# Optimization experiments

Measured on AMD Instinct MI355X. Metric: run time of the kernel, lower is better.

Reference implementation:

```python
import jax, jax.numpy as jnp
import numpy as np

N = 50000   # num nodes
R = 8       # num relations
E = 800000  # num edges
IN, HID, OUT = 128, 128, 64


def rgcn_layer(x, src, dst, etype, W, root, bias):
    """PyG-style RGCNConv: per-relation mean aggregation + root weight + bias.
    x: [N, I], W: [R, I, O], root: [I, O], bias: [O]."""
    O = W.shape[-1]
    # transform node features once per relation: [R, N, O]
    xr = jnp.einsum('ni,rio->rno', x, W)
    # per-edge message = relation-specific transform of source node
    m = xr[etype, src]                      # [E, O] gather
    # mean-aggregate per (relation, dst) pair, then sum over relations
    idx = etype * N + dst                   # combined segment id in [0, R*N)
    s = jax.ops.segment_sum(m, idx, num_segments=R * N)          # [R*N, O]
    c = jax.ops.segment_sum(jnp.ones_like(etype, dtype=m.dtype), idx,
                            num_segments=R * N)                   # [R*N]
    agg = (s / jnp.maximum(c, 1.0)[:, None]).reshape(R, N, O).sum(axis=0)
    return agg + x @ root + bias


def setup_inputs() -> dict:
    key = jax.random.key(0)
    ks = jax.random.split(key, 16)
    x = jax.random.normal(ks[0], (N, IN), dtype=jnp.float32)
    edge_index = jax.random.randint(ks[1], (2, E), 0, N, dtype=jnp.int32)
    edge_type = jax.random.randint(ks[2], (E,), 0, R, dtype=jnp.int32)
    dims = [(IN, HID), (HID, HID), (HID, HID), (HID, OUT)]
    inp = {"x": x, "edge_index": edge_index, "edge_type": edge_type}
    for li, (i, o) in enumerate(dims):
        sc = 1.0 / np.sqrt(i)
        inp[f"W{li+1}"] = jax.random.normal(ks[3 + 3 * li], (R, i, o), dtype=jnp.float32) * sc
        inp[f"root{li+1}"] = jax.random.normal(ks[4 + 3 * li], (i, o), dtype=jnp.float32) * sc
        inp[f"b{li+1}"] = jnp.zeros((o,), dtype=jnp.float32)
    return inp


def reference(x, edge_index, edge_type,
              W1, root1, b1, W2, root2, b2,
              W3, root3, b3, W4, root4, b4):
    src, dst = edge_index[0], edge_index[1]
    h = jax.nn.relu(rgcn_layer(x, src, dst, edge_type, W1, root1, b1))
    h = jax.nn.relu(rgcn_layer(h, src, dst, edge_type, W2, root2, b2))
    h = jax.nn.relu(rgcn_layer(h, src, dst, edge_type, W3, root3, b3))
    h = rgcn_layer(h, src, dst, edge_type, W4, root4, b4)
    return jax.nn.log_softmax(h, axis=1)
```

## Files before the change

### kernel.cpp

```cpp
#include <hip/hip_runtime.h>
#include <math.h>

#define NN 50000
#define RR 8
#define EE 800000
#define RN 400000
#define DIN 128
#define K1 1024
#define KTOT 1152
#define NBLK 391

#define OFF_U    0UL
#define OFF_HB0  102400000UL
#define OFF_HB1  115200000UL
#define OFF_XB   128000000UL
#define OFF_LG   140800000UL
#define OFF_WT   153600000UL
#define OFF_OFFS 154780160UL
#define OFF_CUR  156380288UL
#define OFF_SRT  157980288UL
#define OFF_BS   161180288UL
#define WS_NEED  161184384UL

typedef short bf16x8 __attribute__((ext_vector_type(8)));
typedef float f32x4 __attribute__((ext_vector_type(4)));

__device__ __forceinline__ unsigned f2bf(float f) {
    unsigned x = __float_as_uint(f);
    return (x + 0x7fffu + ((x >> 16) & 1u)) >> 16;
}
__device__ __forceinline__ float bflo(unsigned p) { return __uint_as_float(p << 16); }
__device__ __forceinline__ float bfhi(unsigned p) { return __uint_as_float(p & 0xffff0000u); }

__global__ void k_cvt(const float* __restrict__ x, ushort* __restrict__ xb) {
    int i = blockIdx.x * 256 + threadIdx.x;
    if (i >= NN * 32) return;
    float4 v = ((const float4*)x)[i];
    ushort4 o;
    o.x = (ushort)f2bf(v.x); o.y = (ushort)f2bf(v.y);
    o.z = (ushort)f2bf(v.z); o.w = (ushort)f2bf(v.w);
    ((ushort4*)xb)[i] = o;
}

__global__ void k_wt(const float* __restrict__ W, const float* __restrict__ Rt,
                     ushort* __restrict__ WT, int O) {
    int o = blockIdx.x;
    for (int k = threadIdx.x; k < KTOT; k += 256) {
        float v = (k < K1)
            ? W[(size_t)(k >> 7) * 128 * O + (size_t)(k & 127) * O + o]
            : Rt[(size_t)(k - K1) * O + o];
        WT[(size_t)o * KTOT + k] = (ushort)f2bf(v);
    }
}

__global__ void k_hist(const int* __restrict__ ei, const int* __restrict__ et,
                       int* __restrict__ hist) {
    int e = blockIdx.x * blockDim.x + threadIdx.x;
    if (e >= EE) return;
    atomicAdd(&hist[ei[EE + e] * RR + et[e]], 1);
}

__global__ void k_scan1(const int* __restrict__ hist, int* __restrict__ offs,
                        int* __restrict__ bsums) {
    __shared__ int tmp[1024];
    int tid = threadIdx.x;
    int g = blockIdx.x * 1024 + tid;
    int v = (g < RN) ? hist[g] : 0;
    tmp[tid] = v;
    __syncthreads();
    for (int off = 1; off < 1024; off <<= 1) {
        int t = tmp[tid];
        if (tid >= off) t += tmp[tid - off];
        __syncthreads();
        tmp[tid] = t;
        __syncthreads();
    }
    if (g < RN) offs[g] = tmp[tid] - v;
    if (tid == 1023) bsums[blockIdx.x] = tmp[1023];
}

__global__ void k_scan2(int* __restrict__ bsums) {
    __shared__ int tmp[1024];
    int tid = threadIdx.x;
    int v = (tid < NBLK) ? bsums[tid] : 0;
    tmp[tid] = v;
    __syncthreads();
    for (int off = 1; off < 1024; off <<= 1) {
        int t = tmp[tid];
        if (tid >= off) t += tmp[tid - off];
        __syncthreads();
        tmp[tid] = t;
        __syncthreads();
    }
    if (tid < NBLK) bsums[tid] = tmp[tid] - v;
}

__global__ void k_scan3(int* __restrict__ offs, const int* __restrict__ bsums) {
    int g = blockIdx.x * 1024 + threadIdx.x;
    if (g < RN) offs[g] += bsums[blockIdx.x];
    else if (g == RN) offs[RN] = EE;
}

__global__ void k_scatter(const int* __restrict__ ei, const int* __restrict__ et,
                          const int* __restrict__ offs, int* __restrict__ cur,
                          int* __restrict__ ssrc) {
    int e = blockIdx.x * blockDim.x + threadIdx.x;
    if (e >= EE) return;
    int s = ei[EE + e] * RR + et[e];
    ssrc[offs[s] + atomicAdd(&cur[s], 1)] = ei[e];
}

__global__ __launch_bounds__(256) void k_agg(const ushort* __restrict__ hb,
        const int* __restrict__ offs, const int* __restrict__ ssrc,
        ushort* __restrict__ u) {
    int gt = blockIdx.x * 256 + threadIdx.x;
    int wid = gt >> 6, lane = gt & 63;
    int nw = (gridDim.x * 256) >> 6;
    const unsigned* h2 = (const unsigned*)hb;
    unsigned* u2 = (unsigned*)u;
    for (int s = wid; s < RN; s += nw) {
        int beg = offs[s], end = offs[s + 1];
        float a0 = 0.f, a1 = 0.f;
        int e = beg;
        for (; e + 1 < end; e += 2) {
            int s0 = ssrc[e], s1 = ssrc[e + 1];
            unsigned p0 = h2[s0 * 64 + lane];
            unsigned p1 = h2[s1 * 64 + lane];
            a0 += bflo(p0) + bflo(p1);
            a1 += bfhi(p0) + bfhi(p1);
        }
        if (e < end) {
            unsigned p = h2[ssrc[e] * 64 + lane];
            a0 += bflo(p); a1 += bfhi(p);
        }
        float inv = 1.0f / (float)max(end - beg, 1);
        a0 *= inv; a1 *= inv;
        u2[s * 64 + lane] = f2bf(a0) | (f2bf(a1) << 16);
    }
}

template<int WAVES_M, int WAVES_N, int MT, bool RELU, bool OUTF32>
__global__ __launch_bounds__(256) void k_gemm(
        const ushort* __restrict__ u, const ushort* __restrict__ hb,
        const ushort* __restrict__ WT, const float* __restrict__ bias,
        void* __restrict__ outv) {
    constexpr int BN = WAVES_N * 32;
    __shared__ ushort As[64 * 64];
    const int tid = threadIdx.x;
    const int lane = tid & 63;
    const int w = tid >> 6;
    const int wr = w / WAVES_N;
    const int wc = w % WAVES_N;
    const int m0 = blockIdx.x * 64;
    f32x4 acc[MT][2] = {};

    for (int kt = 0; kt < KTOT; kt += 64) {
        const ushort* base; int rstride, kc;
        if (kt < K1) { base = u;  rstride = 1024; kc = kt; }
        else         { base = hb; rstride = 128;  kc = kt - K1; }
#pragma unroll
        for (int i = 0; i < 2; ++i) {
            int slot = i * 256 + tid;
            int r = slot >> 3, c16 = slot & 7;
            int n = min(m0 + r, NN - 1);
            uint4 v = *(const uint4*)(base + (size_t)n * rstride + kc + c16 * 8);
            *(uint4*)(&As[r * 64 + ((c16 ^ (r & 7)) * 8)]) = v;
        }
        __syncthreads();
#pragma unroll
        for (int kk = 0; kk < 2; ++kk) {
            bf16x8 bfr[2];
#pragma unroll
            for (int nt = 0; nt < 2; ++nt) {
                int col = wc * 32 + nt * 16 + (lane & 15);
                int k = kt + kk * 32 + (lane >> 4) * 8;
                bfr[nt] = *(const bf16x8*)(WT + (size_t)col * KTOT + k);
            }
#pragma unroll
            for (int mt = 0; mt < MT; ++mt) {
                int row = wr * MT * 16 + mt * 16 + (lane & 15);
                int c16 = (kk * 4 + (lane >> 4)) ^ (row & 7);
                bf16x8 a = *(const bf16x8*)(&As[row * 64 + c16 * 8]);
#pragma unroll
                for (int nt = 0; nt < 2; ++nt)
                    acc[mt][nt] = __builtin_amdgcn_mfma_f32_16x16x32_bf16(
                        a, bfr[nt], acc[mt][nt], 0, 0, 0);
            }
        }
        __syncthreads();
    }
#pragma unroll
    for (int mt = 0; mt < MT; ++mt) {
#pragma unroll
        for (int nt = 0; nt < 2; ++nt) {
            int col = wc * 32 + nt * 16 + (lane & 15);
            float bs = bias[col];
#pragma unroll
            for (int j = 0; j < 4; ++j) {
                int row = m0 + wr * MT * 16 + mt * 16 + (lane >> 4) * 4 + j;
                if (row >= NN) continue;
                float v = acc[mt][nt][j] + bs;
                if (RELU) v = fmaxf(v, 0.f);
                if (OUTF32) ((float*)outv)[(size_t)row * BN + col] = v;
                else ((ushort*)outv)[(size_t)row * BN + col] = (ushort)f2bf(v);
            }
        }
    }
}

__global__ void k_logsoftmax(const float* __restrict__ in, float* __restrict__ out) {
    int row = blockIdx.x * 4 + (threadIdx.x >> 6);
    int lane = threadIdx.x & 63;
    if (row >= NN) return;
    float v = in[(size_t)row * 64 + lane];
    float m = v;
#pragma unroll
    for (int off = 32; off; off >>= 1) m = fmaxf(m, __shfl_xor(m, off, 64));
    float e = expf(v - m);
    float s = e;
#pragma unroll
    for (int off = 32; off; off >>= 1) s += __shfl_xor(s, off, 64);
    out[(size_t)row * 64 + lane] = v - m - logf(s);
}

extern "C" void kernel_launch(void* const* d_in, const int* in_sizes, int n_in,
                              void* d_out, int out_size, void* d_ws, size_t ws_size,
                              hipStream_t stream) {
    const float* x  = (const float*)d_in[0];
    const int*   ei = (const int*)d_in[1];
    const int*   et = (const int*)d_in[2];
    const float* W[4]    = {(const float*)d_in[3], (const float*)d_in[6],
                            (const float*)d_in[9], (const float*)d_in[12]};
    const float* root[4] = {(const float*)d_in[4], (const float*)d_in[7],
                            (const float*)d_in[10], (const float*)d_in[13]};
    const float* bias[4] = {(const float*)d_in[5], (const float*)d_in[8],
                            (const float*)d_in[11], (const float*)d_in[14]};

    if (ws_size < WS_NEED) return;

    char* ws = (char*)d_ws;
    ushort* u    = (ushort*)(ws + OFF_U);
    ushort* hb0  = (ushort*)(ws + OFF_HB0);
    ushort* hb1  = (ushort*)(ws + OFF_HB1);
    ushort* xb   = (ushort*)(ws + OFF_XB);
    float*  lg   = (float*)(ws + OFF_LG);
    ushort* WT   = (ushort*)(ws + OFF_WT);
    int*   offs  = (int*)(ws + OFF_OFFS);
    int*   cur   = (int*)(ws + OFF_CUR);
    int*   ssrc  = (int*)(ws + OFF_SRT);
    int*   bsums = (int*)(ws + OFF_BS);
    ushort* WTl[4] = {WT, WT + 147456, WT + 2 * 147456, WT + 3 * 147456};

    k_cvt<<<(NN * 32 + 255) / 256, 256, 0, stream>>>(x, xb);
    k_wt<<<128, 256, 0, stream>>>(W[0], root[0], WTl[0], 128);
    k_wt<<<128, 256, 0, stream>>>(W[1], root[1], WTl[1], 128);
    k_wt<<<128, 256, 0, stream>>>(W[2], root[2], WTl[2], 128);
    k_wt<<<64,  256, 0, stream>>>(W[3], root[3], WTl[3], 64);

    hipMemsetAsync(cur, 0, RN * sizeof(int), stream);
    k_hist<<<(EE + 255) / 256, 256, 0, stream>>>(ei, et, cur);
    k_scan1<<<NBLK, 1024, 0, stream>>>(cur, offs, bsums);
    k_scan2<<<1, 1024, 0, stream>>>(bsums);
    k_scan3<<<NBLK, 1024, 0, stream>>>(offs, bsums);
    hipMemsetAsync(cur, 0, RN * sizeof(int), stream);
    k_scatter<<<(EE + 255) / 256, 256, 0, stream>>>(ei, et, offs, cur, ssrc);

    const int GEMM_G = (NN + 63) / 64;
    k_agg<<<2048, 256, 0, stream>>>(xb, offs, ssrc, u);
    k_gemm<1, 4, 4, true, false><<<GEMM_G, 256, 0, stream>>>(u, xb, WTl[0], bias[0], hb0);
    k_agg<<<2048, 256, 0, stream>>>(hb0, offs, ssrc, u);
    k_gemm<1, 4, 4, true, false><<<GEMM_G, 256, 0, stream>>>(u, hb0, WTl[1], bias[1], hb1);
    k_agg<<<2048, 256, 0, stream>>>(hb1, offs, ssrc, u);
    k_gemm<1, 4, 4, true, false><<<GEMM_G, 256, 0, stream>>>(u, hb1, WTl[2], bias[2], hb0);
    k_agg<<<2048, 256, 0, stream>>>(hb0, offs, ssrc, u);
    k_gemm<2, 2, 2, false, true><<<GEMM_G, 256, 0, stream>>>(u, hb0, WTl[3], bias[3], lg);
    k_logsoftmax<<<(NN + 3) / 4, 256, 0, stream>>>(lg, (float*)d_out);
}
```

Baseline: 601.9 us.

## Fuse per-relation mean aggregation into the GEMM via double-buffered LDS tiles

Replaces the separate aggregation kernel and GEMM with one kernel per layer. Each block gathers and mean-aggregates neighbor features for one relation at a time into a double-buffered LDS tile while running MFMA on the previous relation's tile, then adds the root term read directly from global memory. This removes the write and read of the large [N, R*128] aggregated buffer in global memory and shrinks the workspace. The cost is that aggregation parallelism is now tied to 64-node blocks with 512 threads, and degree imbalance across lanes within a wave can cause divergence stalls.

Result: slower. 943.6 us (+56.8%).

```diff
diff --git a/kernel.cpp b/kernel.cpp
--- a/kernel.cpp
+++ b/kernel.cpp
@@ -10,17 +10,16 @@
 #define KTOT 1152
 #define NBLK 391
 
-#define OFF_U    0UL
-#define OFF_HB0  102400000UL
-#define OFF_HB1  115200000UL
-#define OFF_XB   128000000UL
-#define OFF_LG   140800000UL
-#define OFF_WT   153600000UL
-#define OFF_OFFS 154780160UL
-#define OFF_CUR  156380288UL
-#define OFF_SRT  157980288UL
-#define OFF_BS   161180288UL
-#define WS_NEED  161184384UL
+#define OFF_HB0  0UL
+#define OFF_HB1  12800000UL
+#define OFF_XB   25600000UL
+#define OFF_LG   38400000UL
+#define OFF_WT   51200000UL
+#define OFF_OFFS 52379648UL
+#define OFF_CUR  53979776UL
+#define OFF_SRT  55579776UL
+#define OFF_BS   58779776UL
+#define WS_NEED  58783872UL
 
 typedef short bf16x8 __attribute__((ext_vector_type(8)));
 typedef float f32x4 __attribute__((ext_vector_type(4)));
@@ -110,90 +109,117 @@
     ssrc[offs[s] + atomicAdd(&cur[s], 1)] = ei[e];
 }
 
-__global__ __launch_bounds__(256) void k_agg(const ushort* __restrict__ hb,
-        const int* __restrict__ offs, const int* __restrict__ ssrc,
-        ushort* __restrict__ u) {
-    int gt = blockIdx.x * 256 + threadIdx.x;
-    int wid = gt >> 6, lane = gt & 63;
-    int nw = (gridDim.x * 256) >> 6;
-    const unsigned* h2 = (const unsigned*)hb;
-    unsigned* u2 = (unsigned*)u;
-    for (int s = wid; s < RN; s += nw) {
-        int beg = offs[s], end = offs[s + 1];
-        float a0 = 0.f, a1 = 0.f;
-        int e = beg;
-        for (; e + 1 < end; e += 2) {
-            int s0 = ssrc[e], s1 = ssrc[e + 1];
-            unsigned p0 = h2[s0 * 64 + lane];
-            unsigned p1 = h2[s1 * 64 + lane];
-            a0 += bflo(p0) + bflo(p1);
-            a1 += bfhi(p0) + bfhi(p1);
-        }
-        if (e < end) {
-            unsigned p = h2[ssrc[e] * 64 + lane];
-            a0 += bflo(p); a1 += bfhi(p);
-        }
-        float inv = 1.0f / (float)max(end - beg, 1);
-        a0 *= inv; a1 *= inv;
-        u2[s * 64 + lane] = f2bf(a0) | (f2bf(a1) << 16);
-    }
-}
-
-template<int WAVES_M, int WAVES_N, int MT, bool RELU, bool OUTF32>
-__global__ __launch_bounds__(256) void k_gemm(
-        const ushort* __restrict__ u, const ushort* __restrict__ hb,
-        const ushort* __restrict__ WT, const float* __restrict__ bias,
-        void* __restrict__ outv) {
-    constexpr int BN = WAVES_N * 32;
-    __shared__ ushort As[64 * 64];
+template<int WN, int MT, int NT, bool RELU, bool OUTF32>
+__global__ __launch_bounds__(512, 4) void k_fused(
+        const ushort* __restrict__ hb, const int* __restrict__ offs,
+        const int* __restrict__ ssrc, const ushort* __restrict__ WT,
+        const float* __restrict__ bias, void* __restrict__ outv) {
+    constexpr int BN = WN * NT * 16;
+    __shared__ ushort As[2][64 * 128];
     const int tid = threadIdx.x;
     const int lane = tid & 63;
     const int w = tid >> 6;
-    const int wr = w / WAVES_N;
-    const int wc = w % WAVES_N;
+    const int wr = w / WN;
+    const int wc = w % WN;
     const int m0 = blockIdx.x * 64;
-    f32x4 acc[MT][2] = {};
-
-    for (int kt = 0; kt < KTOT; kt += 64) {
-        const ushort* base; int rstride, kc;
-        if (kt < K1) { base = u;  rstride = 1024; kc = kt; }
-        else         { base = hb; rstride = 128;  kc = kt - K1; }
-#pragma unroll
-        for (int i = 0; i < 2; ++i) {
-            int slot = i * 256 + tid;
-            int r = slot >> 3, c16 = slot & 7;
-            int n = min(m0 + r, NN - 1);
-            uint4 v = *(const uint4*)(base + (size_t)n * rstride + kc + c16 * 8);
-            *(uint4*)(&As[r * 64 + ((c16 ^ (r & 7)) * 8)]) = v;
-        }
-        __syncthreads();
-#pragma unroll
-        for (int kk = 0; kk < 2; ++kk) {
-            bf16x8 bfr[2];
-#pragma unroll
-            for (int nt = 0; nt < 2; ++nt) {
-                int col = wc * 32 + nt * 16 + (lane & 15);
-                int k = kt + kk * 32 + (lane >> 4) * 8;
+    const int half = lane >> 5;
+    const int sub = lane & 31;
+    const uint2* h4 = (const uint2*)hb;
+
+    f32x4 acc[MT][NT] = {};
+
+    auto agg = [&](int r, int buf) {
+        int bg[4], en[4];
+#pragma unroll
+        for (int t = 0; t < 4; ++t) {
+            int node = m0 + w * 8 + 2 * t + half;
+            if (node < NN) {
+                int s = node * 8 + r;
+                bg[t] = offs[s];
+                en[t] = offs[s + 1];
+            } else { bg[t] = 0; en[t] = 0; }
+        }
+#pragma unroll
+        for (int t = 0; t < 4; ++t) {
+            float a0 = 0.f, a1 = 0.f, a2 = 0.f, a3 = 0.f;
+            int e = bg[t], ee = en[t];
+            while (__any(e < ee)) {
+                bool p0 = e < ee, p1 = e + 1 < ee;
+                int i0 = min(e, EE - 1), i1 = min(e + 1, EE - 1);
+                int s0 = ssrc[i0], s1 = ssrc[i1];
+                uint2 q0 = h4[(size_t)s0 * 32 + sub];
+                uint2 q1 = h4[(size_t)s1 * 32 + sub];
+                if (p0) { a0 += bflo(q0.x); a1 += bfhi(q0.x);
+                          a2 += bflo(q0.y); a3 += bfhi(q0.y); }
+                if (p1) { a0 += bflo(q1.x); a1 += bfhi(q1.x);
+                          a2 += bflo(q1.y); a3 += bfhi(q1.y); }
+                e += 2;
+            }
+            float inv = 1.0f / (float)max(en[t] - bg[t], 1);
+            unsigned w0 = f2bf(a0 * inv) | (f2bf(a1 * inv) << 16);
+            unsigned w1 = f2bf(a2 * inv) | (f2bf(a3 * inv) << 16);
+            int row = w * 8 + 2 * t + half;
+            int g = sub >> 1;
+            *(uint2*)(&As[buf][row * 128 + ((g ^ (row & 15)) * 8) + (sub & 1) * 4]) =
+                make_uint2(w0, w1);
+        }
+    };
+
+    auto mma = [&](int p, int buf) {
+#pragma unroll
+        for (int kk = 0; kk < 4; ++kk) {
+            bf16x8 bfr[NT];
+#pragma unroll
+            for (int nt = 0; nt < NT; ++nt) {
+                int col = wc * NT * 16 + nt * 16 + (lane & 15);
+                int k = p * 128 + kk * 32 + (lane >> 4) * 8;
                 bfr[nt] = *(const bf16x8*)(WT + (size_t)col * KTOT + k);
             }
 #pragma unroll
             for (int mt = 0; mt < MT; ++mt) {
                 int row = wr * MT * 16 + mt * 16 + (lane & 15);
-                int c16 = (kk * 4 + (lane >> 4)) ^ (row & 7);
-                bf16x8 a = *(const bf16x8*)(&As[row * 64 + c16 * 8]);
-#pragma unroll
-                for (int nt = 0; nt < 2; ++nt)
+                int g = kk * 4 + (lane >> 4);
+                bf16x8 a = *(const bf16x8*)(&As[buf][row * 128 + ((g ^ (row & 15)) * 8)]);
+#pragma unroll
+                for (int nt = 0; nt < NT; ++nt)
                     acc[mt][nt] = __builtin_amdgcn_mfma_f32_16x16x32_bf16(
                         a, bfr[nt], acc[mt][nt], 0, 0, 0);
             }
         }
-        __syncthreads();
+    };
+
+    agg(0, 0);
+    __syncthreads();
+    for (int p = 0; p < 8; ++p) {
+        mma(p, p & 1);
+        if (p < 7) agg(p + 1, (p + 1) & 1);
+        __syncthreads();
+    }
+#pragma unroll
+    for (int kk = 0; kk < 4; ++kk) {
+        bf16x8 bfr[NT];
+#pragma unroll
+        for (int nt = 0; nt < NT; ++nt) {
+            int col = wc * NT * 16 + nt * 16 + (lane & 15);
+            int k = K1 + kk * 32 + (lane >> 4) * 8;
+            bfr[nt] = *(const bf16x8*)(WT + (size_t)col * KTOT + k);
+        }
+#pragma unroll
+        for (int mt = 0; mt < MT; ++mt) {
+            int row = m0 + wr * MT * 16 + mt * 16 + (lane & 15);
+            int rc = min(row, NN - 1);
+            bf16x8 a = *(const bf16x8*)(hb + (size_t)rc * 128 + kk * 32 + (lane >> 4) * 8);
+#pragma unroll
+            for (int nt = 0; nt < NT; ++nt)
+                acc[mt][nt] = __builtin_amdgcn_mfma_f32_16x16x32_bf16(
+                    a, bfr[nt], acc[mt][nt], 0, 0, 0);
+        }
     }
 #pragma unroll
     for (int mt = 0; mt < MT; ++mt) {
 #pragma unroll
-        for (int nt = 0; nt < 2; ++nt) {
-            int col = wc * 32 + nt * 16 + (lane & 15);
+        for (int nt = 0; nt < NT; ++nt) {
+            int col = wc * NT * 16 + nt * 16 + (lane & 15);
             float bs = bias[col];
 #pragma unroll
             for (int j = 0; j < 4; ++j) {
@@ -239,7 +265,6 @@
     if (ws_size < WS_NEED) return;
 
     char* ws = (char*)d_ws;
-    ushort* u    = (ushort*)(ws + OFF_U);
     ushort* hb0  = (ushort*)(ws + OFF_HB0);
     ushort* hb1  = (ushort*)(ws + OFF_HB1);
     ushort* xb   = (ushort*)(ws + OFF_XB);
@@ -265,14 +290,10 @@
     hipMemsetAsync(cur, 0, RN * sizeof(int), stream);
     k_scatter<<<(EE + 255) / 256, 256, 0, stream>>>(ei, et, offs, cur, ssrc);
 
-    const int GEMM_G = (NN + 63) / 64;
-    k_agg<<<2048, 256, 0, stream>>>(xb, offs, ssrc, u);
-    k_gemm<1, 4, 4, true, false><<<GEMM_G, 256, 0, stream>>>(u, xb, WTl[0], bias[0], hb0);
-    k_agg<<<2048, 256, 0, stream>>>(hb0, offs, ssrc, u);
-    k_gemm<1, 4, 4, true, false><<<GEMM_G, 256, 0, stream>>>(u, hb0, WTl[1], bias[1], hb1);
-    k_agg<<<2048, 256, 0, stream>>>(hb1, offs, ssrc, u);
-    k_gemm<1, 4, 4, true, false><<<GEMM_G, 256, 0, stream>>>(u, hb1, WTl[2], bias[2], hb0);
-    k_agg<<<2048, 256, 0, stream>>>(hb0, offs, ssrc, u);
-    k_gemm<2, 2, 2, false, true><<<GEMM_G, 256, 0, stream>>>(u, hb0, WTl[3], bias[3], lg);
+    const int G = (NN + 63) / 64;
+    k_fused<4, 2, 2, true,  false><<<G, 512, 0, stream>>>(xb,  offs, ssrc, WTl[0], bias[0], hb0);
+    k_fused<4, 2, 2, true,  false><<<G, 512, 0, stream>>>(hb0, offs, ssrc, WTl[1], bias[1], hb1);
+    k_fused<4, 2, 2, true,  false><<<G, 512, 0, stream>>>(hb1, offs, ssrc, WTl[2], bias[2], hb0);
+    k_fused<2, 1, 2, false, true ><<<G, 512, 0, stream>>>(hb0, offs, ssrc, WTl[3], bias[3], lg);
     k_logsoftmax<<<(NN + 3) / 4, 256, 0, stream>>>(lg, (float*)d_out);
 }
```

## Restructure aggregation per node and pipeline GEMM with 128-wide K tiles

Applied to the files above, without the earlier changes.

The aggregation kernel now assigns one wavefront per destination node and handles its 8 relation segments in pairs with half-waves. Source indices are preloaded into lanes and shared via shuffles, and the next node's offsets are prefetched. The GEMM moves from 64-wide to 128-wide K tiles and register-prefetches the next A tile while the MFMAs run, with all four waves splitting N instead of an M/N wave grid. This aims to cut per-segment overhead and barrier count and hide global load latency, in exchange for more registers, more shared memory and wasted lanes on uneven segment lengths.

Measured after the change: 585.9 us. -2.7%, faster.

```diff
diff --git a/kernel.cpp b/kernel.cpp
--- a/kernel.cpp
+++ b/kernel.cpp
@@ -116,88 +116,132 @@
     int gt = blockIdx.x * 256 + threadIdx.x;
     int wid = gt >> 6, lane = gt & 63;
     int nw = (gridDim.x * 256) >> 6;
-    const unsigned* h2 = (const unsigned*)hb;
-    unsigned* u2 = (unsigned*)u;
-    for (int s = wid; s < RN; s += nw) {
-        int beg = offs[s], end = offs[s + 1];
-        float a0 = 0.f, a1 = 0.f;
-        int e = beg;
-        for (; e + 1 < end; e += 2) {
-            int s0 = ssrc[e], s1 = ssrc[e + 1];
-            unsigned p0 = h2[s0 * 64 + lane];
-            unsigned p1 = h2[s1 * 64 + lane];
-            a0 += bflo(p0) + bflo(p1);
-            a1 += bfhi(p0) + bfhi(p1);
-        }
-        if (e < end) {
-            unsigned p = h2[ssrc[e] * 64 + lane];
-            a0 += bflo(p); a1 += bfhi(p);
-        }
-        float inv = 1.0f / (float)max(end - beg, 1);
-        a0 *= inv; a1 *= inv;
-        u2[s * 64 + lane] = f2bf(a0) | (f2bf(a1) << 16);
-    }
-}
-
-template<int WAVES_M, int WAVES_N, int MT, bool RELU, bool OUTF32>
+    int half = lane >> 5;
+    int sub = lane & 31;
+    const uint2* h4 = (const uint2*)hb;
+    uint2* u4 = (uint2*)u;
+
+    if (wid >= NN) return;
+    int b_cur = offs[wid * 8 + min(lane, 8)];
+    for (int n = wid; n < NN; n += nw) {
+        int b0 = __shfl(b_cur, 0);
+        int b8 = __shfl(b_cur, 8);
+        int nb = b8 - b0;
+        int sv = ssrc[min(b0 + min(lane, max(nb - 1, 0)), EE - 1)];
+        int b_nxt = 0;
+        if (n + nw < NN) b_nxt = offs[(n + nw) * 8 + min(lane, 8)];
+#pragma unroll
+        for (int t = 0; t < 4; ++t) {
+            int r = 2 * t + half;
+            int beg = __shfl(b_cur, r);
+            int end = __shfl(b_cur, r + 1);
+            int len = end - beg;
+            int mx = max(__shfl(len, 0), __shfl(len, 32));
+            float a0 = 0.f, a1 = 0.f, a2 = 0.f, a3 = 0.f;
+            for (int j = 0; j < mx; j += 2) {
+                int l0 = beg - b0 + j;
+                int l1 = l0 + 1;
+                int s0 = __shfl(sv, min(l0, 63));
+                int s1 = __shfl(sv, min(l1, 63));
+                if (l1 >= 64) {
+                    s0 = ssrc[min(b0 + l0, EE - 1)];
+                    s1 = ssrc[min(b0 + l1, EE - 1)];
+                }
+                uint2 q0 = h4[(size_t)s0 * 32 + sub];
+                uint2 q1 = h4[(size_t)s1 * 32 + sub];
+                if (j < len) {
+                    a0 += bflo(q0.x); a1 += bfhi(q0.x);
+                    a2 += bflo(q0.y); a3 += bfhi(q0.y);
+                }
+                if (j + 1 < len) {
+                    a0 += bflo(q1.x); a1 += bfhi(q1.x);
+                    a2 += bflo(q1.y); a3 += bfhi(q1.y);
+                }
+            }
+            float inv = 1.0f / (float)max(len, 1);
+            uint2 w;
+            w.x = f2bf(a0 * inv) | (f2bf(a1 * inv) << 16);
+            w.y = f2bf(a2 * inv) | (f2bf(a3 * inv) << 16);
+            u4[(size_t)(n * 8 + r) * 32 + sub] = w;
+        }
+        b_cur = b_nxt;
+    }
+}
+
+template<int NT, bool RELU, bool OUTF32>
 __global__ __launch_bounds__(256) void k_gemm(
         const ushort* __restrict__ u, const ushort* __restrict__ hb,
         const ushort* __restrict__ WT, const float* __restrict__ bias,
         void* __restrict__ outv) {
-    constexpr int BN = WAVES_N * 32;
-    __shared__ ushort As[64 * 64];
+    constexpr int BN = 4 * NT * 16;
+    __shared__ ushort As[64 * 128];
     const int tid = threadIdx.x;
     const int lane = tid & 63;
-    const int w = tid >> 6;
-    const int wr = w / WAVES_N;
-    const int wc = w % WAVES_N;
+    const int wc = tid >> 6;
     const int m0 = blockIdx.x * 64;
-    f32x4 acc[MT][2] = {};
-
-    for (int kt = 0; kt < KTOT; kt += 64) {
-        const ushort* base; int rstride, kc;
-        if (kt < K1) { base = u;  rstride = 1024; kc = kt; }
-        else         { base = hb; rstride = 128;  kc = kt - K1; }
-#pragma unroll
-        for (int i = 0; i < 2; ++i) {
-            int slot = i * 256 + tid;
-            int r = slot >> 3, c16 = slot & 7;
-            int n = min(m0 + r, NN - 1);
-            uint4 v = *(const uint4*)(base + (size_t)n * rstride + kc + c16 * 8);
-            *(uint4*)(&As[r * 64 + ((c16 ^ (r & 7)) * 8)]) = v;
-        }
-        __syncthreads();
-#pragma unroll
-        for (int kk = 0; kk < 2; ++kk) {
-            bf16x8 bfr[2];
-#pragma unroll
-            for (int nt = 0; nt < 2; ++nt) {
-                int col = wc * 32 + nt * 16 + (lane & 15);
-                int k = kt + kk * 32 + (lane >> 4) * 8;
+    f32x4 acc[4][NT] = {};
+    uint4 regs[4];
+
+    auto loadA = [&](int t) {
+#pragma unroll
+        for (int i = 0; i < 4; ++i) {
+            int c = i * 256 + tid;
+            int row = c >> 4, g = c & 15;
+            int nn = min(m0 + row, NN - 1);
+            const ushort* p = (t < 8) ? u + (size_t)nn * 1024 + t * 128 + g * 8
+                                      : hb + (size_t)nn * 128 + g * 8;
+            regs[i] = *(const uint4*)p;
+        }
+    };
+    auto storeA = [&]() {
+#pragma unroll
+        for (int i = 0; i < 4; ++i) {
+            int c = i * 256 + tid;
+            int row = c >> 4, g = c & 15;
+            *(uint4*)(&As[row * 128 + ((g ^ (row & 15)) * 8)]) = regs[i];
+        }
+    };
+    auto mma = [&](int t) {
+#pragma unroll
+        for (int kk = 0; kk < 4; ++kk) {
+            bf16x8 bfr[NT];
+#pragma unroll
+            for (int nt = 0; nt < NT; ++nt) {
+                int col = wc * NT * 16 + nt * 16 + (lane & 15);
+                int k = t * 128 + kk * 32 + (lane >> 4) * 8;
                 bfr[nt] = *(const bf16x8*)(WT + (size_t)col * KTOT + k);
             }
 #pragma unroll
-            for (int mt = 0; mt < MT; ++mt) {
-                int row = wr * MT * 16 + mt * 16 + (lane & 15);
-                int c16 = (kk * 4 + (lane >> 4)) ^ (row & 7);
-                bf16x8 a = *(const bf16x8*)(&As[row * 64 + c16 * 8]);
-#pragma unroll
-                for (int nt = 0; nt < 2; ++nt)
+            for (int mt = 0; mt < 4; ++mt) {
+                int row = mt * 16 + (lane & 15);
+                int g = kk * 4 + (lane >> 4);
+                bf16x8 a = *(const bf16x8*)(&As[row * 128 + ((g ^ (row & 15)) * 8)]);
+#pragma unroll
+                for (int nt = 0; nt < NT; ++nt)
                     acc[mt][nt] = __builtin_amdgcn_mfma_f32_16x16x32_bf16(
                         a, bfr[nt], acc[mt][nt], 0, 0, 0);
             }
         }
-        __syncthreads();
-    }
-#pragma unroll
-    for (int mt = 0; mt < MT; ++mt) {
-#pragma unroll
-        for (int nt = 0; nt < 2; ++nt) {
-            int col = wc * 32 + nt * 16 + (lane & 15);
+    };
+
+    loadA(0);
+    storeA();
+    __syncthreads();
+    for (int t = 0; t < 9; ++t) {
+        if (t + 1 < 9) loadA(t + 1);
+        mma(t);
+        __syncthreads();
+        if (t + 1 < 9) { storeA(); __syncthreads(); }
+    }
+#pragma unroll
+    for (int mt = 0; mt < 4; ++mt) {
+#pragma unroll
+        for (int nt = 0; nt < NT; ++nt) {
+            int col = wc * NT * 16 + nt * 16 + (lane & 15);
             float bs = bias[col];
 #pragma unroll
             for (int j = 0; j < 4; ++j) {
-                int row = m0 + wr * MT * 16 + mt * 16 + (lane >> 4) * 4 + j;
+                int row = m0 + mt * 16 + (lane >> 4) * 4 + j;
                 if (row >= NN) continue;
                 float v = acc[mt][nt][j] + bs;
                 if (RELU) v = fmaxf(v, 0.f);
@@ -265,14 +309,14 @@
     hipMemsetAsync(cur, 0, RN * sizeof(int), stream);
     k_scatter<<<(EE + 255) / 256, 256, 0, stream>>>(ei, et, offs, cur, ssrc);
 
-    const int GEMM_G = (NN + 63) / 64;
+    const int G = (NN + 63) / 64;
     k_agg<<<2048, 256, 0, stream>>>(xb, offs, ssrc, u);
-    k_gemm<1, 4, 4, true, false><<<GEMM_G, 256, 0, stream>>>(u, xb, WTl[0], bias[0], hb0);
+    k_gemm<2, true, false><<<G, 256, 0, stream>>>(u, xb, WTl[0], bias[0], hb0);
     k_agg<<<2048, 256, 0, stream>>>(hb0, offs, ssrc, u);
-    k_gemm<1, 4, 4, true, false><<<GEMM_G, 256, 0, stream>>>(u, hb0, WTl[1], bias[1], hb1);
+    k_gemm<2, true, false><<<G, 256, 0, stream>>>(u, hb0, WTl[1], bias[1], hb1);
     k_agg<<<2048, 256, 0, stream>>>(hb1, offs, ssrc, u);
-    k_gemm<1, 4, 4, true, false><<<GEMM_G, 256, 0, stream>>>(u, hb1, WTl[2], bias[2], hb0);
+    k_gemm<2, true, false><<<G, 256, 0, stream>>>(u, hb1, WTl[2], bias[2], hb0);
     k_agg<<<2048, 256, 0, stream>>>(hb0, offs, ssrc, u);
-    k_gemm<2, 2, 2, false, true><<<GEMM_G, 256, 0, stream>>>(u, hb0, WTl[3], bias[3], lg);
+    k_gemm<1, false, true><<<G, 256, 0, stream>>>(u, hb0, WTl[3], bias[3], lg);
     k_logsoftmax<<<(NN + 3) / 4, 256, 0, stream>>>(lg, (float*)d_out);
 }
```
